# Kernel optimization log

Measured on AMD Instinct MI355X. Metric: run time of the kernel, lower is better.

The kernel has to match this reference:

```python
import jax, jax.numpy as jnp
import numpy as np

N = 8192          # batch_size == number of graph nodes
F1 = 64
F2 = 64
D_IN = F1 * F2    # 4096, = int(sqrt(in_feats))**2
D_OUT = 4096      # out_feats, must equal F1*F2 for the final reshape
ALPHA = 0.2       # LeakyReLU negative slope


def setup_inputs() -> dict:
    key = jax.random.key(0)
    k_x, k_w, k_a = jax.random.split(key, 3)
    x = jax.random.normal(k_x, (N, F1, F2), dtype=jnp.float32)
    # torch Linear weight layout: [out_feats, in_feats]; xavier-uniform-ish scale
    lim_w = float(np.sqrt(6.0 / (D_IN + D_OUT)) * np.sqrt(2.0))
    W = jax.random.uniform(k_w, (D_OUT, D_IN), dtype=jnp.float32, minval=-lim_w, maxval=lim_w)
    lim_a = float(np.sqrt(6.0 / (1 + 2 * D_OUT)))
    a = jax.random.uniform(k_a, (1, 2 * D_OUT), dtype=jnp.float32, minval=-lim_a, maxval=lim_a)
    return {"x": x, "W": W, "a": a}


def reference(x, W, a):
    b, f1, f2 = x.shape
    x_flat = x.reshape(b, f1 * f2)                 # [N, D_in]
    h = x_flat @ W.T                               # [N, D_out]
    # scores[i,j] = leakyrelu(cat(h_i, h_j) @ a.T) = leakyrelu(h_i.a1 + h_j.a2)
    a1 = a[0, :D_OUT]                              # [D_out]
    a2 = a[0, D_OUT:]                              # [D_out]
    s1 = h @ a1                                    # [N]
    s2 = h @ a2                                    # [N]
    e = s1[:, None] + s2[None, :]                  # [N, N]
    e = jnp.where(e > 0, e, ALPHA * e)             # LeakyReLU
    attention = jax.nn.softmax(e, axis=-1)         # [N, N]
    # dropout=0.0 (eval-mode / deterministic reference)
    out = attention @ h                            # [N, D_out]
    return out.reshape(b, f1, f2)
```

## Files before the change

### kernel.cpp

```cpp
#include <hip/hip_runtime.h>
#include <hip/hip_bf16.h>
#include <stdint.h>


typedef float  f32x4  __attribute__((ext_vector_type(4)));
typedef __bf16 bf16x8 __attribute__((ext_vector_type(8)));

#define AS1 __attribute__((address_space(1)))
#define AS3 __attribute__((address_space(3)))

constexpr int NB  = 8192;
constexpr int DF  = 4096;
constexpr int CH  = 64;
constexpr int NCH = NB / CH;

constexpr int GK  = DF;
constexpr int BKK = 64;
constexpr int NT2 = GK / BKK;

__device__ __forceinline__ uint16_t f2bf_u(float f) {
  union { float f; uint32_t u; } x; x.f = f;
  return (uint16_t)((x.u + 0x7FFFu + ((x.u >> 16) & 1u)) >> 16);
}
__device__ __forceinline__ float bfu2f(uint16_t v) {
  union { uint32_t u; float f; } x; x.u = ((uint32_t)v) << 16;
  return x.f;
}

__global__ __launch_bounds__(256) void cvt_all(
    const float* __restrict__ x, uint16_t* __restrict__ xb,
    const float* __restrict__ W, uint16_t* __restrict__ Wb,
    float* __restrict__ z1, float* __restrict__ z2) {
  const int idx = blockIdx.x * 256 + threadIdx.x;
  const int stride = gridDim.x * 256;
  const int n4x = (NB * DF) / 4, n4w = (DF * DF) / 4;
  if (idx < NB) { z1[idx] = 0.f; z2[idx] = 0.f; }
  for (int i = idx; i < n4x; i += stride) {
    float4 v = ((const float4*)x)[i];
    ushort4 o;
    o.x = f2bf_u(v.x); o.y = f2bf_u(v.y); o.z = f2bf_u(v.z); o.w = f2bf_u(v.w);
    ((ushort4*)xb)[i] = o;
  }
  for (int i = idx; i < n4w; i += stride) {
    float4 v = ((const float4*)W)[i];
    ushort4 o;
    o.x = f2bf_u(v.x); o.y = f2bf_u(v.y); o.z = f2bf_u(v.z); o.w = f2bf_u(v.w);
    ((ushort4*)Wb)[i] = o;
  }
}


#define STAGE_A(tt, half) do {                                                 \
  const uint16_t* g0_ = Ag + (size_t)((half) * 128) * GK + (size_t)(tt) * BKK; \
  uint32_t d_ = ((uint32_t)((tt) & 1)) * 32768u + (uint32_t)(half) * 8192u +   \
                (uint32_t)wave * 512u;                                         \
  __builtin_amdgcn_global_load_lds((const AS1 void*)g0_,                       \
      (AS3 void*)(lds + d_), 16, 0, 0);                                        \
  __builtin_amdgcn_global_load_lds((const AS1 void*)(g0_ + (size_t)64 * GK),   \
      (AS3 void*)(lds + d_ + 4096u), 16, 0, 0);                                \
} while (0)

#define STAGE_B(tt, half) do {                                                 \
  const uint16_t* g0_ = Bg + (size_t)((half) * 128) * GK + (size_t)(tt) * BKK; \
  uint32_t d_ = ((uint32_t)((tt) & 1)) * 32768u + 16384u +                     \
                (uint32_t)(half) * 8192u + (uint32_t)wave * 512u;              \
  __builtin_amdgcn_global_load_lds((const AS1 void*)g0_,                       \
      (AS3 void*)(lds + d_), 16, 0, 0);                                        \
  __builtin_amdgcn_global_load_lds((const AS1 void*)(g0_ + (size_t)64 * GK),   \
      (AS3 void*)(lds + d_ + 4096u), 16, 0, 0);                                \
} while (0)

#define LDA(mh) do {                                                           \
  _Pragma("unroll") for (int mf = 0; mf < 4; ++mf)                             \
    _Pragma("unroll") for (int ks = 0; ks < 2; ++ks)                           \
      aF[mf][ks] = *(const bf16x8*)(lds + bufo +                               \
          (uint32_t)(wm * 128 + (mh) * 64 + mf * 16 + lr) * 64u +              \
          (uint32_t)((ks * 32 + lg * 8) ^ swl));                               \
} while (0)

#define LDB(nh) do {                                                           \
  _Pragma("unroll") for (int nf = 0; nf < 2; ++nf)                             \
    _Pragma("unroll") for (int ks = 0; ks < 2; ++ks)                           \
      bF[nf][ks] = *(const bf16x8*)(lds + bufo + 16384u +                      \
          (uint32_t)(wn * 64 + (nh) * 32 + nf * 16 + lr) * 64u +               \
          (uint32_t)((ks * 32 + lg * 8) ^ swl));                               \
} while (0)

#define MMA(mh, nh) do {                                                       \
  _Pragma("unroll") for (int ks = 0; ks < 2; ++ks)                             \
    _Pragma("unroll") for (int mf = 0; mf < 4; ++mf)                           \
      _Pragma("unroll") for (int nf = 0; nf < 2; ++nf)                         \
        acc[(mh) * 4 + mf][(nh) * 2 + nf] =                                    \
            __builtin_amdgcn_mfma_f32_16x16x32_bf16(aF[mf][ks], bF[nf][ks],    \
                acc[(mh) * 4 + mf][(nh) * 2 + nf], 0, 0, 0);                   \
} while (0)

__global__ __launch_bounds__(512, 2) void gemm_nt_async(
    const uint16_t* __restrict__ A, const uint16_t* __restrict__ B,
    uint16_t* __restrict__ C, const float* __restrict__ a,
    float* __restrict__ s1g, float* __restrict__ s2g) {
  __shared__ uint16_t lds[65536];

  const int tid  = threadIdx.x;
  const int wave = tid >> 6;
  const int lane = tid & 63;
  const int lr   = lane & 15;
  const int lg   = lane >> 4;
  const int wm   = wave >> 2;
  const int wn   = wave & 3;
  const int swl  = (lr & 7) << 3;

  const int bid = blockIdx.x;
  const int swz = (bid & 7) * 64 + (bid >> 3);
  const int bx  = swz & 15;
  const int by  = swz >> 4;
  const int rowBase = by * 256;
  const int colBase = bx * 256;

  const int sr  = tid >> 3;
  const int sch = (tid & 7) ^ (sr & 7);
  const uint16_t* Ag = A + (size_t)(rowBase + sr) * GK + sch * 8;
  const uint16_t* Bg = B + (size_t)(colBase + sr) * GK + sch * 8;

  f32x4 acc[8][4];
#pragma unroll
  for (int mf = 0; mf < 8; ++mf)
#pragma unroll
    for (int nf = 0; nf < 4; ++nf) acc[mf][nf] = (f32x4){0.f, 0.f, 0.f, 0.f};

  STAGE_A(0, 0);
  STAGE_A(0, 1);
  STAGE_B(0, 0);
  STAGE_B(0, 1);
  asm volatile("s_waitcnt vmcnt(0)" ::: "memory");
  __builtin_amdgcn_s_barrier();

  bf16x8 aF[4][2], bF[2][2];

  for (int t = 0; t < NT2; ++t) {
    const uint32_t bufo = ((uint32_t)(t & 1)) * 32768u;

    if (t + 1 < NT2) {
      STAGE_A(t + 1, 0);
      STAGE_A(t + 1, 1);
      STAGE_B(t + 1, 0);
      STAGE_B(t + 1, 1);
    }

    LDA(0); LDB(0);
    MMA(0, 0);
    LDB(1);
    MMA(0, 1);
    LDA(1);
    MMA(1, 1);
    LDB(0);
    MMA(1, 0);

    if (t + 1 < NT2) {
      asm volatile("s_waitcnt vmcnt(0)" ::: "memory");
      __builtin_amdgcn_s_barrier();
    }
  }

  const int r0 = rowBase + wm * 128 + lg * 4;
  const int c0 = colBase + wn * 64 + lr;
#pragma unroll
  for (int mf = 0; mf < 8; ++mf)
#pragma unroll
    for (int nf = 0; nf < 4; ++nf)
#pragma unroll
      for (int e = 0; e < 4; ++e)
        C[(size_t)(r0 + mf * 16 + e) * (size_t)DF + (c0 + nf * 16)] =
            f2bf_u(acc[mf][nf][e]);

  float a1v[4], a2v[4];
#pragma unroll
  for (int nf = 0; nf < 4; ++nf) {
    int col = c0 + nf * 16;
    a1v[nf] = a[col];
    a2v[nf] = a[DF + col];
  }
  float* sP = (float*)lds;
#pragma unroll
  for (int mf = 0; mf < 8; ++mf) {
#pragma unroll
    for (int e = 0; e < 4; ++e) {
      float p1 = 0.f, p2 = 0.f;
#pragma unroll
      for (int nf = 0; nf < 4; ++nf) {
        float hv = acc[mf][nf][e];
        p1 += hv * a1v[nf];
        p2 += hv * a2v[nf];
      }
      p1 += __shfl_xor(p1, 1, 64); p1 += __shfl_xor(p1, 2, 64);
      p1 += __shfl_xor(p1, 4, 64); p1 += __shfl_xor(p1, 8, 64);
      p2 += __shfl_xor(p2, 1, 64); p2 += __shfl_xor(p2, 2, 64);
      p2 += __shfl_xor(p2, 4, 64); p2 += __shfl_xor(p2, 8, 64);
      if (lr == 0) {
        int rl = wm * 128 + lg * 4 + mf * 16 + e;
        sP[wn * 256 + rl]        = p1;
        sP[1024 + wn * 256 + rl] = p2;
      }
    }
  }
  __syncthreads();
  if (tid < 256) {
    float v1 = sP[tid] + sP[256 + tid] + sP[512 + tid] + sP[768 + tid];
    float v2 = sP[1024 + tid] + sP[1280 + tid] + sP[1536 + tid] + sP[1792 + tid];
    atomicAdd(&s1g[rowBase + tid], v1);
    atomicAdd(&s2g[rowBase + tid], v2);
  }
}

__global__ __launch_bounds__(256) void rankcount_kernel(
    const float* __restrict__ s1, const float* __restrict__ s2,
    int* __restrict__ pi, float* __restrict__ s2sorted, int* __restrict__ ci,
    float* __restrict__ wbg, float* __restrict__ wcg) {
  __shared__ float ld[NB];
  const int t   = threadIdx.x;
  const int bid = blockIdx.x;
  for (int idx = t; idx < NB; idx += 256) ld[idx] = s2[idx];
  __syncthreads();
  const int i = bid * 64 + (t >> 2);
  const int p = t & 3;
  const float v   = ld[i];
  const float thr = -s1[i];
  int cr = 0, cc = 0;
  const int q0 = p * (NB / 16);
  for (int it = 0; it < NB / 16; it++) {
    int qq = q0 + ((it + p) & (NB / 16 - 1));
    float4 u = ((const float4*)ld)[qq];
    int jj = qq * 4;
    cr += (u.x > v) || (u.x == v && (jj + 0) < i);
    cr += (u.y > v) || (u.y == v && (jj + 1) < i);
    cr += (u.z > v) || (u.z == v && (jj + 2) < i);
    cr += (u.w > v) || (u.w == v && (jj + 3) < i);
    cc += (u.x > thr) + (u.y > thr) + (u.z > thr) + (u.w > thr);
  }
  cr += __shfl_xor(cr, 1, 64); cr += __shfl_xor(cr, 2, 64);
  cc += __shfl_xor(cc, 1, 64); cc += __shfl_xor(cc, 2, 64);
  if (p == 0) {
    pi[cr] = i;
    s2sorted[cr] = v;
    ci[i] = cc;
    wbg[cr] = __expf(0.2f * v);
    wcg[cr] = __expf(v);
  }
}

union MpSmem {
  struct { float pb[256]; float pc[256]; int histL[NB + 1]; int ps[256]; } mg;
  struct { int pj[CH]; float wb[CH]; float wc[CH]; } pp;
};

__global__ __launch_bounds__(256) void megapass1_kernel(
    const uint16_t* __restrict__ h, const int* __restrict__ pi,
    const float* __restrict__ wbg, const float* __restrict__ wcg,
    const float* __restrict__ s1, const int* __restrict__ ci,
    float* __restrict__ Sb, float* __restrict__ Sc,
    float* __restrict__ f1, float* __restrict__ f2,
    int* __restrict__ istart, int* __restrict__ ilist,
    float* __restrict__ Bct, float* __restrict__ Cct) {
  __shared__ MpSmem smu;
  const int t   = threadIdx.x;
  const int bid = blockIdx.x;

  if (bid == 0) {
    for (int g = t; g <= NB; g += 256) smu.mg.histL[g] = 0;
    float sb = 0.f, sc = 0.f;
    for (int c = t * 32; c < t * 32 + 32; c++) { sb += wbg[c]; sc += wcg[c]; }
    smu.mg.pb[t] = sb; smu.mg.pc[t] = sc;
    __syncthreads();
    if (t == 0) {
      float rb = 0.f, rc = 0.f;
      for (int q = 0; q < 256; q++) {
        float tb = smu.mg.pb[q], tc = smu.mg.pc[q];
        smu.mg.pb[q] = rb; smu.mg.pc[q] = rc;
        rb += tb; rc += tc;
      }
      Sb[0] = 0.f; Sc[0] = 0.f;
      Sb[NB] = rb; Sc[NB] = rc;
    }
    __syncthreads();
    {
      float rb = smu.mg.pb[t], rc = smu.mg.pc[t];
      for (int c = t * 32; c < t * 32 + 32; c++) {
        rb += wbg[c]; rc += wcg[c];
        if (c + 1 < NB) { Sb[c + 1] = rb; Sc[c + 1] = rc; }
      }
    }
    __syncthreads();
    const float SbT = Sb[NB];
    for (int qq = 0; qq < NB / 256; qq++) {
      int i = qq * 256 + t;
      float s1i = s1[i];
      int c = ci[i];
      float q1 = __expf(0.2f * s1i), q2 = __expf(s1i);
      float l = q1 * (SbT - Sb[c]) + q2 * Sc[c];
      f1[i] = q1 / l;
      f2[i] = q2 / l;
      atomicAdd(&smu.mg.histL[c], 1);
    }
    __syncthreads();
    {
      const int lo = t * 33;
      const int hi = min(lo + 33, NB + 1);
      int s = 0;
      for (int b = lo; b < hi; b++) s += smu.mg.histL[b];
      smu.mg.ps[t] = s;
      __syncthreads();
      if (t == 0) {
        int r = 0;
        for (int q = 0; q < 256; q++) {
          int v = smu.mg.ps[q]; smu.mg.ps[q] = r; r += v;
        }
      }
      __syncthreads();
      int r = smu.mg.ps[t];
      for (int b = lo; b < hi; b++) {
        istart[b] = r;
        int hv = smu.mg.histL[b];
        smu.mg.histL[b] = r;
        r += hv;
      }
      if (t == 255) istart[NB + 1] = r;
    }
    __syncthreads();
    for (int qq = 0; qq < NB / 256; qq++) {
      int i = qq * 256 + t;
      int pos = atomicAdd(&smu.mg.histL[ci[i]], 1);
      ilist[pos] = i;
    }
    return;
  }

  const int fb = bid - 1;
  const int cb = fb & 3;
  const int k  = fb >> 2;
  if (t < CH) {
    int g = k * CH + t;
    smu.pp.pj[t] = pi[g]; smu.pp.wb[t] = wbg[g]; smu.pp.wc[t] = wcg[g];
  }
  __syncthreads();
  const int n0 = cb * 1024 + t * 4;
  float b0 = 0.f, b1 = 0.f, b2 = 0.f, b3 = 0.f;
  float c0 = 0.f, c1 = 0.f, c2 = 0.f, c3 = 0.f;
#pragma unroll 8
  for (int c = 0; c < CH; c++) {
    uint2 hv = *(const uint2*)(h + (size_t)smu.pp.pj[c] * DF + n0);
    float h0 = bfu2f((uint16_t)hv.x), h1 = bfu2f((uint16_t)(hv.x >> 16));
    float h2 = bfu2f((uint16_t)hv.y), h3 = bfu2f((uint16_t)(hv.y >> 16));
    float vb = smu.pp.wb[c], vc = smu.pp.wc[c];
    b0 += vb * h0; b1 += vb * h1; b2 += vb * h2; b3 += vb * h3;
    c0 += vc * h0; c1 += vc * h1; c2 += vc * h2; c3 += vc * h3;
  }
  *(float4*)(Bct + (size_t)k * DF + n0) = make_float4(b0, b1, b2, b3);
  *(float4*)(Cct + (size_t)k * DF + n0) = make_float4(c0, c1, c2, c3);
}

__global__ __launch_bounds__(256) void boff_kernel(
    const float* __restrict__ Bct, const float* __restrict__ Cct,
    float* __restrict__ Boff, float* __restrict__ Coff) {
  __shared__ float sB[4][64], sC[4][64];
  const int t   = threadIdx.x;
  const int cl  = t & 63;
  const int seg = t >> 6;
  const int col = blockIdx.x * 64 + cl;
  float sb = 0.f, sc = 0.f;
#pragma unroll 8
  for (int u = 0; u < NCH / 4; u++) {
    int kk = seg * (NCH / 4) + u;
    sb += Bct[(size_t)kk * DF + col];
    sc += Cct[(size_t)kk * DF + col];
  }
  sB[seg][cl] = sb; sC[seg][cl] = sc;
  __syncthreads();
  float rb = 0.f, rc = 0.f;
#pragma unroll
  for (int s = 0; s < 3; s++)
    if (s < seg) { rb += sB[s][cl]; rc += sC[s][cl]; }
#pragma unroll 4
  for (int u = 0; u < NCH / 4; u++) {
    int kk = seg * (NCH / 4) + u;
    Boff[(size_t)kk * DF + col] = rb;
    Coff[(size_t)kk * DF + col] = rc;
    rb += Bct[(size_t)kk * DF + col];
    rc += Cct[(size_t)kk * DF + col];
  }
  if (seg == 3) {
    Boff[(size_t)NCH * DF + col] = rb;
    Coff[(size_t)NCH * DF + col] = rc;
  }
}

__global__ __launch_bounds__(256) void pass2_kernel(
    const uint16_t* __restrict__ h, const int* __restrict__ pi,
    const float* __restrict__ wbg, const float* __restrict__ wcg,
    const float* __restrict__ Boff, const float* __restrict__ Coff,
    const int* __restrict__ istart, const int* __restrict__ ilist,
    const float* __restrict__ f1, const float* __restrict__ f2,
    float* __restrict__ out) {
  __shared__ int   pj[CH];
  __shared__ float wb[CH], wc[CH];
  __shared__ int   se[CH + 2];
  const int t  = threadIdx.x;
  const int cb = blockIdx.x;
  const int k  = blockIdx.y;
  if (t < CH) {
    int g = k * CH + t;
    pj[t] = pi[g]; wb[t] = wbg[g]; wc[t] = wcg[g];
  }
  if (t < CH + 2) se[t] = istart[k * CH + t];
  __syncthreads();
  const int n0 = cb * 1024 + t * 4;
  const float4 An = *(const float4*)(Boff + (size_t)NCH * DF + n0);
  const float4 Bo = *(const float4*)(Boff + (size_t)k * DF + n0);
  const float4 Co = *(const float4*)(Coff + (size_t)k * DF + n0);
  float b0 = Bo.x, b1 = Bo.y, b2 = Bo.z, b3 = Bo.w;
  float c0 = Co.x, c1 = Co.y, c2 = Co.z, c3 = Co.w;

  if (k == 0) {
    for (int idx = se[0]; idx < se[1]; idx++) {
      const int i = ilist[idx];
      const float fa = f1[i];
      *(float4*)(out + (size_t)i * DF + n0) =
          make_float4(fa * An.x, fa * An.y, fa * An.z, fa * An.w);
    }
  }
  for (int c = 0; c < CH; c++) {
    uint2 hv = *(const uint2*)(h + (size_t)pj[c] * DF + n0);
    float h0 = bfu2f((uint16_t)hv.x), h1 = bfu2f((uint16_t)(hv.x >> 16));
    float h2 = bfu2f((uint16_t)hv.y), h3 = bfu2f((uint16_t)(hv.y >> 16));
    float vb = wb[c], vc = wc[c];
    b0 += vb * h0; b1 += vb * h1; b2 += vb * h2; b3 += vb * h3;
    c0 += vc * h0; c1 += vc * h1; c2 += vc * h2; c3 += vc * h3;
    const int e0 = se[c + 1], e1 = se[c + 2];
    for (int idx = e0; idx < e1; idx++) {
      const int i = ilist[idx];
      const float fa = f1[i], fb = f2[i];
      *(float4*)(out + (size_t)i * DF + n0) = make_float4(
          fa * (An.x - b0) + fb * c0, fa * (An.y - b1) + fb * c1,
          fa * (An.z - b2) + fb * c2, fa * (An.w - b3) + fb * c3);
    }
  }
}

extern "C" void kernel_launch(void* const* d_in, const int* in_sizes, int n_in,
                              void* d_out, int out_size, void* d_ws, size_t ws_size,
                              hipStream_t stream) {
  const float* x = (const float*)d_in[0];
  const float* W = (const float*)d_in[1];
  const float* a = (const float*)d_in[2];
  float* out = (float*)d_out;

  char* ws = (char*)d_ws;
  uint16_t* h = (uint16_t*)ws;
  char* sm = ws + 67108864;
  float* s1       = (float*)(sm);
  float* s2       = (float*)(sm + 65536);
  float* s2sorted = (float*)(sm + 131072);
  int*   pi       = (int*)  (sm + 196608);
  int*   ci       = (int*)  (sm + 262144);
  float* Sb       = (float*)(sm + 327680);
  float* Sc       = (float*)(sm + 393216);
  float* wbg      = (float*)(sm + 458752);
  float* wcg      = (float*)(sm + 524288);
  float* f1       = (float*)(sm + 589824);
  float* f2       = (float*)(sm + 655360);
  int*   istart   = (int*)  (sm + 786432);
  int*   ilist    = (int*)  (sm + 917504);
  float* Bct      = (float*)(sm + 1048576);
  float* Cct      = (float*)(sm + 3145728);
  float* Boff     = (float*)(sm + 5242880);
  float* Coff     = (float*)(sm + 7602176);
  char* base2 = ws + 67108864 + 10485760;
  uint16_t* xb = (uint16_t*)base2;
  uint16_t* Wb = (uint16_t*)(base2 + 67108864);

  cvt_all<<<1024, 256, 0, stream>>>(x, xb, W, Wb, s1, s2);

  gemm_nt_async<<<(NB / 256) * (DF / 256), 512, 0, stream>>>(
      xb, Wb, h, a, s1, s2);

  rankcount_kernel<<<NB / 64, 256, 0, stream>>>(
      s1, s2, pi, s2sorted, ci, wbg, wcg);

  megapass1_kernel<<<1 + (DF / 1024) * NCH, 256, 0, stream>>>(
      h, pi, wbg, wcg, s1, ci, Sb, Sc, f1, f2, istart, ilist, Bct, Cct);

  boff_kernel<<<DF / 64, 256, 0, stream>>>(Bct, Cct, Boff, Coff);

  pass2_kernel<<<dim3(DF / 1024, NCH), 256, 0, stream>>>(
      h, pi, wbg, wcg, Boff, Coff, istart, ilist, f1, f2, out);
}
```

Before: 747.6 us.

## Fuse post-GEMM kernels pairwise using ticket ordering and global spin barriers

```diff
diff --git a/kernel.cpp b/kernel.cpp
--- a/kernel.cpp
+++ b/kernel.cpp
@@ -30,11 +30,12 @@
 __global__ __launch_bounds__(256) void cvt_all(
     const float* __restrict__ x, uint16_t* __restrict__ xb,
     const float* __restrict__ W, uint16_t* __restrict__ Wb,
-    float* __restrict__ z1, float* __restrict__ z2) {
+    float* __restrict__ z1, float* __restrict__ z2, int* __restrict__ tk) {
   const int idx = blockIdx.x * 256 + threadIdx.x;
   const int stride = gridDim.x * 256;
   const int n4x = (NB * DF) / 4, n4w = (DF * DF) / 4;
   if (idx < NB) { z1[idx] = 0.f; z2[idx] = 0.f; }
+  if (idx < 4) tk[idx] = 0;
   for (int i = idx; i < n4x; i += stride) {
     float4 v = ((const float4*)x)[i];
     ushort4 o;
@@ -48,7 +49,6 @@
     ((ushort4*)Wb)[i] = o;
   }
 }
-
 
 #define STAGE_A(tt, half) do {                                                 \
   const uint16_t* g0_ = Ag + (size_t)((half) * 128) * GK + (size_t)(tt) * BKK; \
@@ -212,60 +212,84 @@
   }
 }
 
-__global__ __launch_bounds__(256) void rankcount_kernel(
-    const float* __restrict__ s1, const float* __restrict__ s2,
-    int* __restrict__ pi, float* __restrict__ s2sorted, int* __restrict__ ci,
-    float* __restrict__ wbg, float* __restrict__ wcg) {
-  __shared__ float ld[NB];
-  const int t   = threadIdx.x;
-  const int bid = blockIdx.x;
-  for (int idx = t; idx < NB; idx += 256) ld[idx] = s2[idx];
-  __syncthreads();
-  const int i = bid * 64 + (t >> 2);
-  const int p = t & 3;
-  const float v   = ld[i];
-  const float thr = -s1[i];
-  int cr = 0, cc = 0;
-  const int q0 = p * (NB / 16);
-  for (int it = 0; it < NB / 16; it++) {
-    int qq = q0 + ((it + p) & (NB / 16 - 1));
-    float4 u = ((const float4*)ld)[qq];
-    int jj = qq * 4;
-    cr += (u.x > v) || (u.x == v && (jj + 0) < i);
-    cr += (u.y > v) || (u.y == v && (jj + 1) < i);
-    cr += (u.z > v) || (u.z == v && (jj + 2) < i);
-    cr += (u.w > v) || (u.w == v && (jj + 3) < i);
-    cc += (u.x > thr) + (u.y > thr) + (u.z > thr) + (u.w > thr);
-  }
-  cr += __shfl_xor(cr, 1, 64); cr += __shfl_xor(cr, 2, 64);
-  cc += __shfl_xor(cc, 1, 64); cc += __shfl_xor(cc, 2, 64);
-  if (p == 0) {
-    pi[cr] = i;
-    s2sorted[cr] = v;
-    ci[i] = cc;
-    wbg[cr] = __expf(0.2f * v);
-    wcg[cr] = __expf(v);
-  }
-}
-
-union MpSmem {
+__device__ __forceinline__ int take_ticket(int* tk, int* lds_slot) {
+  if (threadIdx.x == 0)
+    *lds_slot = __hip_atomic_fetch_add(tk, 1, __ATOMIC_RELAXED,
+                                       __HIP_MEMORY_SCOPE_AGENT);
+  __syncthreads();
+  return *lds_slot;
+}
+__device__ __forceinline__ void release_done(int* done) {
+  __syncthreads();
+  __threadfence();
+  if (threadIdx.x == 0)
+    __hip_atomic_fetch_add(done, 1, __ATOMIC_RELEASE, __HIP_MEMORY_SCOPE_AGENT);
+}
+__device__ __forceinline__ void acquire_spin(int* done, int target) {
+  if (threadIdx.x == 0) {
+    while (__hip_atomic_load(done, __ATOMIC_ACQUIRE,
+                             __HIP_MEMORY_SCOPE_AGENT) < target)
+      __builtin_amdgcn_s_sleep(8);
+  }
+  __syncthreads();
+  __threadfence();
+}
+
+union RcSmem {
+  float ld[NB];
   struct { float pb[256]; float pc[256]; int histL[NB + 1]; int ps[256]; } mg;
   struct { int pj[CH]; float wb[CH]; float wc[CH]; } pp;
 };
 
-__global__ __launch_bounds__(256) void megapass1_kernel(
-    const uint16_t* __restrict__ h, const int* __restrict__ pi,
-    const float* __restrict__ wbg, const float* __restrict__ wcg,
-    const float* __restrict__ s1, const int* __restrict__ ci,
+__global__ __launch_bounds__(256) void rcmp1_kernel(
+    const uint16_t* __restrict__ h,
+    const float* __restrict__ s1, const float* __restrict__ s2,
+    int* __restrict__ pi, float* __restrict__ s2sorted, int* __restrict__ ci,
+    float* __restrict__ wbg, float* __restrict__ wcg,
     float* __restrict__ Sb, float* __restrict__ Sc,
     float* __restrict__ f1, float* __restrict__ f2,
     int* __restrict__ istart, int* __restrict__ ilist,
-    float* __restrict__ Bct, float* __restrict__ Cct) {
-  __shared__ MpSmem smu;
-  const int t   = threadIdx.x;
-  const int bid = blockIdx.x;
-
-  if (bid == 0) {
+    float* __restrict__ Bct, float* __restrict__ Cct,
+    int* __restrict__ tk) {
+  __shared__ RcSmem smu;
+  __shared__ int tslot;
+  const int t = threadIdx.x;
+  const int T = take_ticket(&tk[0], &tslot);
+
+  if (T < 128) {
+    for (int idx = t; idx < NB; idx += 256) smu.ld[idx] = s2[idx];
+    __syncthreads();
+    const int i = T * 64 + (t >> 2);
+    const int p = t & 3;
+    const float v   = smu.ld[i];
+    const float thr = -s1[i];
+    int cr = 0, cc = 0;
+    const int q0 = p * (NB / 16);
+    for (int it = 0; it < NB / 16; it++) {
+      int qq = q0 + ((it + p) & (NB / 16 - 1));
+      float4 u = ((const float4*)smu.ld)[qq];
+      int jj = qq * 4;
+      cr += (u.x > v) || (u.x == v && (jj + 0) < i);
+      cr += (u.y > v) || (u.y == v && (jj + 1) < i);
+      cr += (u.z > v) || (u.z == v && (jj + 2) < i);
+      cr += (u.w > v) || (u.w == v && (jj + 3) < i);
+      cc += (u.x > thr) + (u.y > thr) + (u.z > thr) + (u.w > thr);
+    }
+    cr += __shfl_xor(cr, 1, 64); cr += __shfl_xor(cr, 2, 64);
+    cc += __shfl_xor(cc, 1, 64); cc += __shfl_xor(cc, 2, 64);
+    if (p == 0) {
+      pi[cr] = i;
+      s2sorted[cr] = v;
+      ci[i] = cc;
+      wbg[cr] = __expf(0.2f * v);
+      wcg[cr] = __expf(v);
+    }
+    release_done(&tk[1]);
+  }
+
+  acquire_spin(&tk[1], 128);
+
+  if (T == 128) {
     for (int g = t; g <= NB; g += 256) smu.mg.histL[g] = 0;
     float sb = 0.f, sc = 0.f;
     for (int c = t * 32; c < t * 32 + 32; c++) { sb += wbg[c]; sc += wcg[c]; }
@@ -334,9 +358,10 @@
     return;
   }
 
-  const int fb = bid - 1;
+  const int fb = (T < 128) ? T : (T - 1);
   const int cb = fb & 3;
   const int k  = fb >> 2;
+  __syncthreads();
   if (t < CH) {
     int g = k * CH + t;
     smu.pp.pj[t] = pi[g]; smu.pp.wb[t] = wbg[g]; smu.pp.wc[t] = wcg[g];
@@ -358,59 +383,66 @@
   *(float4*)(Cct + (size_t)k * DF + n0) = make_float4(c0, c1, c2, c3);
 }
 
-__global__ __launch_bounds__(256) void boff_kernel(
-    const float* __restrict__ Bct, const float* __restrict__ Cct,
-    float* __restrict__ Boff, float* __restrict__ Coff) {
-  __shared__ float sB[4][64], sC[4][64];
-  const int t   = threadIdx.x;
-  const int cl  = t & 63;
-  const int seg = t >> 6;
-  const int col = blockIdx.x * 64 + cl;
-  float sb = 0.f, sc = 0.f;
-#pragma unroll 8
-  for (int u = 0; u < NCH / 4; u++) {
-    int kk = seg * (NCH / 4) + u;
-    sb += Bct[(size_t)kk * DF + col];
-    sc += Cct[(size_t)kk * DF + col];
-  }
-  sB[seg][cl] = sb; sC[seg][cl] = sc;
-  __syncthreads();
-  float rb = 0.f, rc = 0.f;
-#pragma unroll
-  for (int s = 0; s < 3; s++)
-    if (s < seg) { rb += sB[s][cl]; rc += sC[s][cl]; }
-#pragma unroll 4
-  for (int u = 0; u < NCH / 4; u++) {
-    int kk = seg * (NCH / 4) + u;
-    Boff[(size_t)kk * DF + col] = rb;
-    Coff[(size_t)kk * DF + col] = rc;
-    rb += Bct[(size_t)kk * DF + col];
-    rc += Cct[(size_t)kk * DF + col];
-  }
-  if (seg == 3) {
-    Boff[(size_t)NCH * DF + col] = rb;
-    Coff[(size_t)NCH * DF + col] = rc;
-  }
-}
-
-__global__ __launch_bounds__(256) void pass2_kernel(
+union BfSmem {
+  struct { float sB[4][64]; float sC[4][64]; } bo;
+  struct { int pj[CH]; float wb[CH]; float wc[CH]; int se[CH + 2]; } pp;
+};
+
+__global__ __launch_bounds__(256) void bfp2_kernel(
     const uint16_t* __restrict__ h, const int* __restrict__ pi,
     const float* __restrict__ wbg, const float* __restrict__ wcg,
-    const float* __restrict__ Boff, const float* __restrict__ Coff,
+    const float* __restrict__ Bct, const float* __restrict__ Cct,
+    float* __restrict__ Boff, float* __restrict__ Coff,
     const int* __restrict__ istart, const int* __restrict__ ilist,
     const float* __restrict__ f1, const float* __restrict__ f2,
-    float* __restrict__ out) {
-  __shared__ int   pj[CH];
-  __shared__ float wb[CH], wc[CH];
-  __shared__ int   se[CH + 2];
-  const int t  = threadIdx.x;
-  const int cb = blockIdx.x;
-  const int k  = blockIdx.y;
+    float* __restrict__ out, int* __restrict__ tk) {
+  __shared__ BfSmem smu;
+  __shared__ int tslot;
+  const int t = threadIdx.x;
+  const int T = take_ticket(&tk[2], &tslot);
+
+  if (T < 64) {
+    const int cl  = t & 63;
+    const int seg = t >> 6;
+    const int col = T * 64 + cl;
+    float sb = 0.f, sc = 0.f;
+#pragma unroll 8
+    for (int u = 0; u < NCH / 4; u++) {
+      int kk = seg * (NCH / 4) + u;
+      sb += Bct[(size_t)kk * DF + col];
+      sc += Cct[(size_t)kk * DF + col];
+    }
+    smu.bo.sB[seg][cl] = sb; smu.bo.sC[seg][cl] = sc;
+    __syncthreads();
+    float rb = 0.f, rc = 0.f;
+#pragma unroll
+    for (int s = 0; s < 3; s++)
+      if (s < seg) { rb += smu.bo.sB[s][cl]; rc += smu.bo.sC[s][cl]; }
+#pragma unroll 4
+    for (int u = 0; u < NCH / 4; u++) {
+      int kk = seg * (NCH / 4) + u;
+      Boff[(size_t)kk * DF + col] = rb;
+      Coff[(size_t)kk * DF + col] = rc;
+      rb += Bct[(size_t)kk * DF + col];
+      rc += Cct[(size_t)kk * DF + col];
+    }
+    if (seg == 3) {
+      Boff[(size_t)NCH * DF + col] = rb;
+      Coff[(size_t)NCH * DF + col] = rc;
+    }
+    release_done(&tk[3]);
+  }
+
+  acquire_spin(&tk[3], 64);
+
+  const int cb = T & 3;
+  const int k  = T >> 2;
+  __syncthreads();
   if (t < CH) {
     int g = k * CH + t;
-    pj[t] = pi[g]; wb[t] = wbg[g]; wc[t] = wcg[g];
-  }
-  if (t < CH + 2) se[t] = istart[k * CH + t];
+    smu.pp.pj[t] = pi[g]; smu.pp.wb[t] = wbg[g]; smu.pp.wc[t] = wcg[g];
+  }
+  if (t < CH + 2) smu.pp.se[t] = istart[k * CH + t];
   __syncthreads();
   const int n0 = cb * 1024 + t * 4;
   const float4 An = *(const float4*)(Boff + (size_t)NCH * DF + n0);
@@ -420,7 +452,7 @@
   float c0 = Co.x, c1 = Co.y, c2 = Co.z, c3 = Co.w;
 
   if (k == 0) {
-    for (int idx = se[0]; idx < se[1]; idx++) {
+    for (int idx = smu.pp.se[0]; idx < smu.pp.se[1]; idx++) {
       const int i = ilist[idx];
       const float fa = f1[i];
       *(float4*)(out + (size_t)i * DF + n0) =
@@ -428,13 +460,13 @@
     }
   }
   for (int c = 0; c < CH; c++) {
-    uint2 hv = *(const uint2*)(h + (size_t)pj[c] * DF + n0);
+    uint2 hv = *(const uint2*)(h + (size_t)smu.pp.pj[c] * DF + n0);
     float h0 = bfu2f((uint16_t)hv.x), h1 = bfu2f((uint16_t)(hv.x >> 16));
     float h2 = bfu2f((uint16_t)hv.y), h3 = bfu2f((uint16_t)(hv.y >> 16));
-    float vb = wb[c], vc = wc[c];
+    float vb = smu.pp.wb[c], vc = smu.pp.wc[c];
     b0 += vb * h0; b1 += vb * h1; b2 += vb * h2; b3 += vb * h3;
     c0 += vc * h0; c1 += vc * h1; c2 += vc * h2; c3 += vc * h3;
-    const int e0 = se[c + 1], e1 = se[c + 2];
+    const int e0 = smu.pp.se[c + 1], e1 = smu.pp.se[c + 2];
     for (int idx = e0; idx < e1; idx++) {
       const int i = ilist[idx];
       const float fa = f1[i], fb = f2[i];
@@ -467,6 +499,7 @@
   float* wcg      = (float*)(sm + 524288);
   float* f1       = (float*)(sm + 589824);
   float* f2       = (float*)(sm + 655360);
+  int*   tk       = (int*)  (sm + 720896);
   int*   istart   = (int*)  (sm + 786432);
   int*   ilist    = (int*)  (sm + 917504);
   float* Bct      = (float*)(sm + 1048576);
@@ -477,19 +510,15 @@
   uint16_t* xb = (uint16_t*)base2;
   uint16_t* Wb = (uint16_t*)(base2 + 67108864);
 
-  cvt_all<<<1024, 256, 0, stream>>>(x, xb, W, Wb, s1, s2);
+  cvt_all<<<1024, 256, 0, stream>>>(x, xb, W, Wb, s1, s2, tk);
 
   gemm_nt_async<<<(NB / 256) * (DF / 256), 512, 0, stream>>>(
       xb, Wb, h, a, s1, s2);
 
-  rankcount_kernel<<<NB / 64, 256, 0, stream>>>(
-      s1, s2, pi, s2sorted, ci, wbg, wcg);
-
-  megapass1_kernel<<<1 + (DF / 1024) * NCH, 256, 0, stream>>>(
-      h, pi, wbg, wcg, s1, ci, Sb, Sc, f1, f2, istart, ilist, Bct, Cct);
-
-  boff_kernel<<<DF / 64, 256, 0, stream>>>(Bct, Cct, Boff, Coff);
-
-  pass2_kernel<<<dim3(DF / 1024, NCH), 256, 0, stream>>>(
-      h, pi, wbg, wcg, Boff, Coff, istart, ilist, f1, f2, out);
-}
+  rcmp1_kernel<<<513, 256, 0, stream>>>(
+      h, s1, s2, pi, s2sorted, ci, wbg, wcg, Sb, Sc, f1, f2,
+      istart, ilist, Bct, Cct, tk);
+
+  bfp2_kernel<<<512, 256, 0, stream>>>(
+      h, pi, wbg, wcg, Bct, Cct, Boff, Coff, istart, ilist, f1, f2, out, tk);
+}
```

Measured after the change: 955.6 us. 1.28x slower.
